# Optimization experiments

Hardware: AMD Instinct MI355X
Metric: run time of the kernel (lower is better)

Reference implementation:

```python
import jax, jax.numpy as jnp
import numpy as np

N = 100000
E = 1600000
D = 256

def setup_inputs() -> dict:
    key = jax.random.key(0)
    k1, k2, k3 = jax.random.split(key, 3)
    nodes = jax.random.normal(k1, (N, D), dtype=jnp.float32)
    edge_index = jax.random.randint(k2, (2, E), 0, N, dtype=jnp.int64)
    W = jax.random.normal(k3, (D, D), dtype=jnp.float32) * 0.05  # GCN lin weight [out,in]
    b = jnp.zeros((D,), dtype=jnp.float32)
    gamma = jnp.ones((D,), dtype=jnp.float32)
    beta = jnp.zeros((D,), dtype=jnp.float32)
    return {"nodes": nodes, "edge_index": edge_index, "W": W, "b": b,
            "gamma": gamma, "beta": beta}

def reference(nodes, edge_index, W, b, gamma, beta):
    n = nodes.shape[0]
    loop = jnp.arange(n, dtype=edge_index.dtype)
    src = jnp.concatenate([edge_index[0], loop])  # add self-loops (PyG default)
    dst = jnp.concatenate([edge_index[1], loop])
    # linear transform
    x = nodes @ W.T  # [N, D]
    # symmetric normalization: deg from target index, weight 1 per edge
    deg = jnp.zeros((n,), dtype=x.dtype).at[dst].add(1.0)
    dinv = jnp.where(deg > 0, jax.lax.rsqrt(deg), 0.0)
    norm = dinv[src] * dinv[dst]  # [E+N]
    msg = x[src] * norm[:, None]
    out = jax.ops.segment_sum(msg, dst, num_segments=n) + b  # [N, D]
    # LayerNorm over feature dim
    mu = jnp.mean(out, axis=-1, keepdims=True)
    var = jnp.mean(jnp.square(out - mu), axis=-1, keepdims=True)
    out = (out - mu) * jax.lax.rsqrt(var + 1e-5) * gamma + beta
    # ReLU; dropout is identity in eval mode
    return jax.nn.relu(out)
```

## Files before the change

### kernel.cpp

```cpp
#include <hip/hip_runtime.h>
#include <hip/hip_bf16.h>

#define NN 100000
#define EE 1600000
#define DD 256
#define CAP 64
#define NPART 391
#define ABLK 512
#define ACHUNK 3125

typedef __bf16 bf16x8 __attribute__((ext_vector_type(8)));
typedef float f32x4 __attribute__((ext_vector_type(4)));

__device__ __forceinline__ unsigned short f2bf(float f) {
    unsigned u = __builtin_bit_cast(unsigned, f);
    u += 0x7fffu + ((u >> 16) & 1u);
    return (unsigned short)(u >> 16);
}
__device__ __forceinline__ float bf2f(unsigned short h) {
    unsigned u = ((unsigned)h) << 16;
    return __builtin_bit_cast(float, u);
}

__global__ __launch_bounds__(256) void k_partA(const void* __restrict__ eptr,
        unsigned int* __restrict__ gseg2, int* __restrict__ cnts, int* __restrict__ pref) {
    __shared__ int lcnt[NPART];
    __shared__ int lcnt2[NPART];
    __shared__ int lpref[NPART];
    __shared__ int sA[512], sB[512];
    __shared__ int lflag;
    const int b = blockIdx.x, tid = threadIdx.x;
    if (tid == 0) lflag = 0;
    for (int i = tid; i < NPART; i += 256) { lcnt[i] = 0; lcnt2[i] = 0; }
    __syncthreads();
    if (tid < 64) {
        const unsigned long long w = ((const unsigned long long*)eptr)[tid];
        if (w > 0xFFFFFFFFULL) lflag = 1;
    }
    __syncthreads();
    const int is32 = lflag;
    const int e0 = b * ACHUNK;
    for (int e = e0 + tid; e < e0 + ACHUNK; e += 256) {
        const int d = is32 ? ((const int*)eptr)[EE + e]
                           : (int)((const long long*)eptr)[EE + e];
        atomicAdd(&lcnt[d >> 8], 1);
    }
    __syncthreads();
    sA[tid]       = (tid < NPART) ? lcnt[tid] : 0;
    sA[tid + 256] = (tid + 256 < NPART) ? lcnt[tid + 256] : 0;
    __syncthreads();
    int* s = sA; int* d2 = sB;
    for (int off = 1; off < 512; off <<= 1) {
        d2[tid]       = s[tid]       + (tid >= off ? s[tid - off] : 0);
        d2[tid + 256] = s[tid + 256] + (tid + 256 >= off ? s[tid + 256 - off] : 0);
        __syncthreads();
        int* t = s; s = d2; d2 = t;
    }
    for (int i = tid; i < NPART; i += 256) {
        lpref[i] = (i == 0) ? 0 : s[i - 1];
        cnts[(size_t)i * ABLK + b] = lcnt[i];
        pref[(size_t)i * ABLK + b] = (i == 0) ? 0 : s[i - 1];
    }
    __syncthreads();
    for (int e = e0 + tid; e < e0 + ACHUNK; e += 256) {
        int ss, dd;
        if (is32) { const int* p = (const int*)eptr; ss = p[e]; dd = p[EE + e]; }
        else { const long long* p = (const long long*)eptr; ss = (int)p[e]; dd = (int)p[EE + e]; }
        const int pp = dd >> 8;
        const int slot = atomicAdd(&lcnt2[pp], 1);
        gseg2[(size_t)b * ACHUNK + lpref[pp] + slot] = ((unsigned)ss << 8) | (unsigned)(dd & 255);
    }
}

__global__ __launch_bounds__(256) void k_partB(const unsigned int* __restrict__ gseg2,
        const int* __restrict__ cnts, const int* __restrict__ pref,
        int* __restrict__ bucket, int* __restrict__ cnt) {
    __shared__ int lc[256];
    __shared__ __align__(16) int lb[256 * CAP];
    const int p = blockIdx.x, tid = threadIdx.x;
    const int node0 = p * 256 + tid;
    lc[tid] = 1;
    lb[tid * CAP] = node0;
    __syncthreads();
    #pragma unroll
    for (int half = 0; half < 2; ++half) {
        const int bb = half * 256 + tid;
        const int c = cnts[(size_t)p * ABLK + bb];
        const unsigned int* seg = gseg2 + (size_t)bb * ACHUNK + pref[(size_t)p * ABLK + bb];
        for (int i = 0; i < c; ++i) {
            const unsigned int en = seg[i];
            const int d = en & 255;
            const int slot = atomicAdd(&lc[d], 1);
            if (slot < CAP) lb[d * CAP + slot] = (int)(en >> 8);
        }
    }
    __syncthreads();
    const size_t base = (size_t)p * 256 * CAP;
    #pragma unroll
    for (int it = 0; it < 16; ++it) {
        const int idx4 = it * 256 + tid;
        const int node = p * 256 + (idx4 >> 4);
        if (node < NN)
            *(uint4*)(bucket + base + (size_t)idx4 * 4) = *(const uint4*)&lb[idx4 * 4];
    }
    if (node0 < NN) cnt[node0] = lc[tid];
}

__global__ void k_detect(const unsigned long long* __restrict__ e64, int* __restrict__ flag) {
    if (threadIdx.x == 0 && blockIdx.x == 0) {
        int is32 = 0;
        for (int i = 0; i < 64; ++i)
            if (e64[i] > 0xFFFFFFFFULL) is32 = 1;
        *flag = is32;
    }
}
__global__ __launch_bounds__(256) void k_init(int* __restrict__ cnt, int* __restrict__ bucket) {
    int v = blockIdx.x * 256 + threadIdx.x;
    if (v < NN) { cnt[v] = 1; bucket[(size_t)v * CAP] = v; }
}
__global__ __launch_bounds__(256) void k_count_scatter(const void* __restrict__ eptr,
        const int* __restrict__ flag, int* __restrict__ cnt, int* __restrict__ bucket) {
    int e = blockIdx.x * 256 + threadIdx.x;
    if (e >= EE) return;
    int s, d;
    if (*flag) { const int* p = (const int*)eptr; s = p[e]; d = p[EE + e]; }
    else { const long long* p = (const long long*)eptr; s = (int)p[e]; d = (int)p[EE + e]; }
    int slot = atomicAdd(&cnt[d], 1);
    if (slot < CAP) bucket[(size_t)d * CAP + slot] = s;
}

__global__ __launch_bounds__(256) void k_wconv(const float* __restrict__ W,
        unsigned short* __restrict__ wf) {
    const int s = blockIdx.x * 256 + threadIdx.x;
    const int lane = s & 63;
    const int ks = (s >> 6) & 7;
    const int g  = (s >> 9) & 3;
    const int wv = s >> 11;
    const int feat = wv * 64 + g * 16 + (lane & 15);
    const int k0 = ks * 32 + (lane >> 4) * 8;
    const float* wp = W + (size_t)feat * 256 + k0;
    unsigned short o[8];
    #pragma unroll
    for (int j = 0; j < 8; ++j) o[j] = f2bf(wp[j]);
    uint4 pk;
    pk.x = o[0] | ((unsigned)o[1] << 16); pk.y = o[2] | ((unsigned)o[3] << 16);
    pk.z = o[4] | ((unsigned)o[5] << 16); pk.w = o[6] | ((unsigned)o[7] << 16);
    *(uint4*)(wf + (size_t)s * 8) = pk;
}

__global__ __launch_bounds__(256) void k_gemm(const float* __restrict__ nodes,
        const unsigned short* __restrict__ wf, const int* __restrict__ cnt,
        unsigned short* __restrict__ y) {
    __shared__ __align__(16) unsigned short xlds[64][264];
    const int tid = threadIdx.x, lane = tid & 63, wv = tid >> 6;
    const int q = lane >> 4, n0 = lane & 15;

    bf16x8 afrag[8][4];
    #pragma unroll
    for (int g = 0; g < 4; ++g)
        #pragma unroll
        for (int ks = 0; ks < 8; ++ks)
            afrag[ks][g] = *(const bf16x8*)(wf + ((((size_t)wv * 4 + g) * 8 + ks) * 64 + lane) * 8);

    const int row0 = blockIdx.x * 64;
    #pragma unroll
    for (int rr = 0; rr < 16; ++rr) {
        const int idx = rr * 256 + tid;
        const int r = idx >> 6, c4 = idx & 63;
        const int grow = min(row0 + r, NN - 1);
        const float4 v = *(const float4*)(nodes + (size_t)grow * 256 + c4 * 4);
        uint2 pk;
        pk.x = (unsigned)f2bf(v.x) | ((unsigned)f2bf(v.y) << 16);
        pk.y = (unsigned)f2bf(v.z) | ((unsigned)f2bf(v.w) << 16);
        *(uint2*)&xlds[r][c4 * 4] = pk;
    }
    __syncthreads();

    #pragma unroll
    for (int sub = 0; sub < 4; ++sub) {
        f32x4 acc[4] = {{0,0,0,0},{0,0,0,0},{0,0,0,0},{0,0,0,0}};
        #pragma unroll
        for (int ks = 0; ks < 8; ++ks) {
            const bf16x8 xf = *(const bf16x8*)&xlds[sub * 16 + n0][ks * 32 + q * 8];
            #pragma unroll
            for (int g = 0; g < 4; ++g)
                acc[g] = __builtin_amdgcn_mfma_f32_16x16x32_bf16(afrag[ks][g], xf, acc[g], 0, 0, 0);
        }
        const int node = row0 + sub * 16 + n0;
        if (node < NN) {
            const float dval = rsqrtf((float)cnt[node]);
            unsigned short* yp = y + (size_t)node * 256 + wv * 64 + q * 4;
            #pragma unroll
            for (int g = 0; g < 4; ++g) {
                uint2 pk;
                pk.x = (unsigned)f2bf(acc[g][0] * dval) | ((unsigned)f2bf(acc[g][1] * dval) << 16);
                pk.y = (unsigned)f2bf(acc[g][2] * dval) | ((unsigned)f2bf(acc[g][3] * dval) << 16);
                *(uint2*)(yp + g * 16) = pk;
            }
        }
    }
}

__global__ __launch_bounds__(256) void k_gather(const unsigned short* __restrict__ y,
        const int* __restrict__ cnt, const int* __restrict__ bucket,
        const float* __restrict__ bias, const float* __restrict__ gamma,
        const float* __restrict__ beta, float* __restrict__ out) {
    const int v = blockIdx.x * 4 + (threadIdx.x >> 6);
    const int lane = threadIdx.x & 63;
    const int h = lane >> 5, l = lane & 31;
    const int c = cnt[v];
    const int m = min(c, CAP);
    const int my = (lane < m) ? bucket[(size_t)v * CAP + lane] : 0;

    float acc[8] = {0, 0, 0, 0, 0, 0, 0, 0};
    #define ACCUM(P) do {                                                   \
        acc[0] += bf2f((unsigned short)((P).x & 0xffff));                   \
        acc[1] += bf2f((unsigned short)((P).x >> 16));                      \
        acc[2] += bf2f((unsigned short)((P).y & 0xffff));                   \
        acc[3] += bf2f((unsigned short)((P).y >> 16));                      \
        acc[4] += bf2f((unsigned short)((P).z & 0xffff));                   \
        acc[5] += bf2f((unsigned short)((P).z >> 16));                      \
        acc[6] += bf2f((unsigned short)((P).w & 0xffff));                   \
        acc[7] += bf2f((unsigned short)((P).w >> 16));                      \
    } while (0)

    int j = 0;
    for (; j + 8 <= m; j += 8) {
        const int s0 = __shfl(my, j + h);
        const int s1 = __shfl(my, j + 2 + h);
        const int s2 = __shfl(my, j + 4 + h);
        const int s3 = __shfl(my, j + 6 + h);
        const uint4 p0 = *((const uint4*)(y + (size_t)s0 * 256) + l);
        const uint4 p1 = *((const uint4*)(y + (size_t)s1 * 256) + l);
        const uint4 p2 = *((const uint4*)(y + (size_t)s2 * 256) + l);
        const uint4 p3 = *((const uint4*)(y + (size_t)s3 * 256) + l);
        ACCUM(p0); ACCUM(p1); ACCUM(p2); ACCUM(p3);
    }
    for (; j + 4 <= m; j += 4) {
        const int s0 = __shfl(my, j + h);
        const int s1 = __shfl(my, j + 2 + h);
        const uint4 p0 = *((const uint4*)(y + (size_t)s0 * 256) + l);
        const uint4 p1 = *((const uint4*)(y + (size_t)s1 * 256) + l);
        ACCUM(p0); ACCUM(p1);
    }
    for (; j + 2 <= m; j += 2) {
        const int s0 = __shfl(my, j + h);
        const uint4 p0 = *((const uint4*)(y + (size_t)s0 * 256) + l);
        ACCUM(p0);
    }
    if (j < m) {
        const int st = __shfl(my, j);
        if (h == 0) {
            const uint4 p0 = *((const uint4*)(y + (size_t)st * 256) + l);
            ACCUM(p0);
        }
    }
    #undef ACCUM

    #pragma unroll
    for (int i = 0; i < 8; ++i) acc[i] += __shfl_xor(acc[i], 32);

    const float dvv = rsqrtf((float)c);
    const float4 b0 = *(const float4*)(bias + l * 8);
    const float4 b1 = *(const float4*)(bias + l * 8 + 4);
    float u[8];
    u[0] = acc[0] * dvv + b0.x; u[1] = acc[1] * dvv + b0.y;
    u[2] = acc[2] * dvv + b0.z; u[3] = acc[3] * dvv + b0.w;
    u[4] = acc[4] * dvv + b1.x; u[5] = acc[5] * dvv + b1.y;
    u[6] = acc[6] * dvv + b1.z; u[7] = acc[7] * dvv + b1.w;

    float s1 = 0, s2 = 0;
    #pragma unroll
    for (int i = 0; i < 8; ++i) { s1 += u[i]; s2 += u[i] * u[i]; }
    #pragma unroll
    for (int o = 16; o > 0; o >>= 1) {
        s1 += __shfl_xor(s1, o);
        s2 += __shfl_xor(s2, o);
    }
    const float mean = s1 * (1.0f / 256.0f);
    const float var  = s2 * (1.0f / 256.0f) - mean * mean;
    const float rstd = rsqrtf(var + 1e-5f);

    const float4 g0 = *(const float4*)(gamma + l * 8);
    const float4 g1 = *(const float4*)(gamma + l * 8 + 4);
    const float4 e0 = *(const float4*)(beta + l * 8);
    const float4 e1 = *(const float4*)(beta + l * 8 + 4);
    float o8[8];
    o8[0] = fmaxf(0.0f, (u[0] - mean) * rstd * g0.x + e0.x);
    o8[1] = fmaxf(0.0f, (u[1] - mean) * rstd * g0.y + e0.y);
    o8[2] = fmaxf(0.0f, (u[2] - mean) * rstd * g0.z + e0.z);
    o8[3] = fmaxf(0.0f, (u[3] - mean) * rstd * g0.w + e0.w);
    o8[4] = fmaxf(0.0f, (u[4] - mean) * rstd * g1.x + e1.x);
    o8[5] = fmaxf(0.0f, (u[5] - mean) * rstd * g1.y + e1.y);
    o8[6] = fmaxf(0.0f, (u[6] - mean) * rstd * g1.z + e1.z);
    o8[7] = fmaxf(0.0f, (u[7] - mean) * rstd * g1.w + e1.w);
    float4 ov;
    if (h == 0) { ov.x = o8[0]; ov.y = o8[1]; ov.z = o8[2]; ov.w = o8[3]; }
    else        { ov.x = o8[4]; ov.y = o8[5]; ov.z = o8[6]; ov.w = o8[7]; }
    *(float4*)(out + (size_t)v * 256 + l * 8 + h * 4) = ov;
}

extern "C" void kernel_launch(void* const* d_in, const int* in_sizes, int n_in,
                              void* d_out, int out_size, void* d_ws, size_t ws_size,
                              hipStream_t stream) {
    const float* nodes = (const float*)d_in[0];
    const void*  edges = d_in[1];
    const float* W     = (const float*)d_in[2];
    const float* b     = (const float*)d_in[3];
    const float* gamma = (const float*)d_in[4];
    const float* beta  = (const float*)d_in[5];
    float* out = (float*)d_out;

    char* ws = (char*)d_ws;
    size_t off = 0;
    auto alloc = [&](size_t bytes) { size_t p = off; off = (off + bytes + 255) & ~(size_t)255; return p; };
    int*            cnt    = (int*)(ws + alloc((size_t)NN * 4));
    int*            flag   = (int*)(ws + alloc(256));
    int*            bucket = (int*)(ws + alloc((size_t)NN * CAP * 4));
    unsigned short* y      = (unsigned short*)(ws + alloc((size_t)NN * DD * 2));
    unsigned short* wf     = (unsigned short*)(ws + alloc((size_t)DD * DD * 2));
    int*            cnts   = (int*)(ws + alloc((size_t)NPART * ABLK * 4));
    int*            pref   = (int*)(ws + alloc((size_t)NPART * ABLK * 4));
    unsigned int*   gseg2  = (unsigned int*)(ws + alloc((size_t)EE * 4));
    const size_t full_need = off;
    (void)in_sizes; (void)n_in; (void)out_size;

    k_wconv<<<32, 256, 0, stream>>>(W, wf);
    if (ws_size >= full_need) {
        k_partA<<<ABLK, 256, 0, stream>>>(edges, gseg2, cnts, pref);
        k_partB<<<NPART, 256, 0, stream>>>(gseg2, cnts, pref, bucket, cnt);
    } else {
        k_detect<<<1, 64, 0, stream>>>((const unsigned long long*)edges, flag);
        k_init<<<(NN + 255) / 256, 256, 0, stream>>>(cnt, bucket);
        k_count_scatter<<<(EE + 255) / 256, 256, 0, stream>>>(edges, flag, cnt, bucket);
    }
    k_gemm<<<(NN + 63) / 64, 256, 0, stream>>>(nodes, wf, cnt, y);
    k_gather<<<NN / 4, 256, 0, stream>>>(y, cnt, bucket, b, gamma, beta, out);
}
```

Baseline: 374.5 us.

## Replace two-pass edge partition with global counting sort by destination partition

Splits the edge bucketing into histogram, column scan, partition prefix scan, sorted scatter, and per-partition bucket fill. Each partition's edges now sit contiguously, so bucket blocks read them with all threads striding coalesced. Before, each thread walked its own small per-chunk segment serially. Adds three kernel launches and a serial column scan of 512 steps per partition, and re-reads the edge list in the sort pass. Block indices are also remapped to chunks so that concurrently running blocks cover different parts of the edge array.

```diff
diff --git a/kernel.cpp b/kernel.cpp
--- a/kernel.cpp
+++ b/kernel.cpp
@@ -21,17 +21,15 @@
     unsigned u = ((unsigned)h) << 16;
     return __builtin_bit_cast(float, u);
 }
-
-__global__ __launch_bounds__(256) void k_partA(const void* __restrict__ eptr,
-        unsigned int* __restrict__ gseg2, int* __restrict__ cnts, int* __restrict__ pref) {
+__device__ __forceinline__ int chunk_of_block(int g) { return (g & 7) * 64 + (g >> 3); }
+
+__global__ __launch_bounds__(256) void k_hist(const void* __restrict__ eptr,
+        int* __restrict__ cnts ) {
     __shared__ int lcnt[NPART];
-    __shared__ int lcnt2[NPART];
-    __shared__ int lpref[NPART];
-    __shared__ int sA[512], sB[512];
     __shared__ int lflag;
-    const int b = blockIdx.x, tid = threadIdx.x;
+    const int b = chunk_of_block(blockIdx.x), tid = threadIdx.x;
     if (tid == 0) lflag = 0;
-    for (int i = tid; i < NPART; i += 256) { lcnt[i] = 0; lcnt2[i] = 0; }
+    for (int i = tid; i < NPART; i += 256) lcnt[i] = 0;
     __syncthreads();
     if (tid < 64) {
         const unsigned long long w = ((const unsigned long long*)eptr)[tid];
@@ -46,35 +44,68 @@
         atomicAdd(&lcnt[d >> 8], 1);
     }
     __syncthreads();
-    sA[tid]       = (tid < NPART) ? lcnt[tid] : 0;
-    sA[tid + 256] = (tid + 256 < NPART) ? lcnt[tid + 256] : 0;
-    __syncthreads();
-    int* s = sA; int* d2 = sB;
+    for (int i = tid; i < NPART; i += 256) cnts[(size_t)b * NPART + i] = lcnt[i];
+}
+
+__global__ __launch_bounds__(256) void k_colscan(const int* __restrict__ cnts,
+        int* __restrict__ gbase , int* __restrict__ T) {
+    const int p = blockIdx.x * 256 + threadIdx.x;
+    if (p >= NPART) return;
+    int run = 0;
+    #pragma unroll 8
+    for (int b = 0; b < ABLK; ++b) {
+        const int v = cnts[(size_t)b * NPART + p];
+        gbase[(size_t)b * NPART + p] = run;
+        run += v;
+    }
+    T[p] = run;
+}
+
+__global__ __launch_bounds__(512) void k_pscan(const int* __restrict__ T, int* __restrict__ P) {
+    __shared__ int sA[512], sB[512];
+    const int tid = threadIdx.x;
+    sA[tid] = (tid < NPART) ? T[tid] : 0;
+    __syncthreads();
+    int* s = sA; int* d = sB;
     for (int off = 1; off < 512; off <<= 1) {
-        d2[tid]       = s[tid]       + (tid >= off ? s[tid - off] : 0);
-        d2[tid + 256] = s[tid + 256] + (tid + 256 >= off ? s[tid + 256 - off] : 0);
+        d[tid] = s[tid] + (tid >= off ? s[tid - off] : 0);
         __syncthreads();
-        int* t = s; s = d2; d2 = t;
-    }
+        int* t = s; s = d; d = t;
+    }
+    if (tid <= NPART) P[tid] = (tid == 0) ? 0 : s[tid - 1];
+}
+
+__global__ __launch_bounds__(256) void k_sortwrite(const void* __restrict__ eptr,
+        const int* __restrict__ gbase, const int* __restrict__ P,
+        unsigned int* __restrict__ sorted) {
+    __shared__ int lc[NPART], gb[NPART];
+    __shared__ int lflag;
+    const int b = chunk_of_block(blockIdx.x), tid = threadIdx.x;
+    if (tid == 0) lflag = 0;
     for (int i = tid; i < NPART; i += 256) {
-        lpref[i] = (i == 0) ? 0 : s[i - 1];
-        cnts[(size_t)i * ABLK + b] = lcnt[i];
-        pref[(size_t)i * ABLK + b] = (i == 0) ? 0 : s[i - 1];
-    }
-    __syncthreads();
+        lc[i] = 0;
+        gb[i] = gbase[(size_t)b * NPART + i] + P[i];
+    }
+    __syncthreads();
+    if (tid < 64) {
+        const unsigned long long w = ((const unsigned long long*)eptr)[tid];
+        if (w > 0xFFFFFFFFULL) lflag = 1;
+    }
+    __syncthreads();
+    const int is32 = lflag;
+    const int e0 = b * ACHUNK;
     for (int e = e0 + tid; e < e0 + ACHUNK; e += 256) {
         int ss, dd;
         if (is32) { const int* p = (const int*)eptr; ss = p[e]; dd = p[EE + e]; }
         else { const long long* p = (const long long*)eptr; ss = (int)p[e]; dd = (int)p[EE + e]; }
         const int pp = dd >> 8;
-        const int slot = atomicAdd(&lcnt2[pp], 1);
-        gseg2[(size_t)b * ACHUNK + lpref[pp] + slot] = ((unsigned)ss << 8) | (unsigned)(dd & 255);
-    }
-}
-
-__global__ __launch_bounds__(256) void k_partB(const unsigned int* __restrict__ gseg2,
-        const int* __restrict__ cnts, const int* __restrict__ pref,
-        int* __restrict__ bucket, int* __restrict__ cnt) {
+        const int slot = atomicAdd(&lc[pp], 1);
+        sorted[gb[pp] + slot] = ((unsigned)ss << 8) | (unsigned)(dd & 255);
+    }
+}
+
+__global__ __launch_bounds__(256) void k_bucket(const unsigned int* __restrict__ sorted,
+        const int* __restrict__ P, int* __restrict__ bucket, int* __restrict__ cnt) {
     __shared__ int lc[256];
     __shared__ __align__(16) int lb[256 * CAP];
     const int p = blockIdx.x, tid = threadIdx.x;
@@ -82,17 +113,12 @@
     lc[tid] = 1;
     lb[tid * CAP] = node0;
     __syncthreads();
-    #pragma unroll
-    for (int half = 0; half < 2; ++half) {
-        const int bb = half * 256 + tid;
-        const int c = cnts[(size_t)p * ABLK + bb];
-        const unsigned int* seg = gseg2 + (size_t)bb * ACHUNK + pref[(size_t)p * ABLK + bb];
-        for (int i = 0; i < c; ++i) {
-            const unsigned int en = seg[i];
-            const int d = en & 255;
-            const int slot = atomicAdd(&lc[d], 1);
-            if (slot < CAP) lb[d * CAP + slot] = (int)(en >> 8);
-        }
+    const int start = P[p], end = P[p + 1];
+    for (int i = start + tid; i < end; i += 256) {
+        const unsigned int en = sorted[i];
+        const int d = en & 255;
+        const int slot = atomicAdd(&lc[d], 1);
+        if (slot < CAP) lb[d * CAP + slot] = (int)(en >> 8);
     }
     __syncthreads();
     const size_t base = (size_t)p * 256 * CAP;
@@ -319,16 +345,21 @@
     int*            bucket = (int*)(ws + alloc((size_t)NN * CAP * 4));
     unsigned short* y      = (unsigned short*)(ws + alloc((size_t)NN * DD * 2));
     unsigned short* wf     = (unsigned short*)(ws + alloc((size_t)DD * DD * 2));
-    int*            cnts   = (int*)(ws + alloc((size_t)NPART * ABLK * 4));
-    int*            pref   = (int*)(ws + alloc((size_t)NPART * ABLK * 4));
-    unsigned int*   gseg2  = (unsigned int*)(ws + alloc((size_t)EE * 4));
+    int*            cnts   = (int*)(ws + alloc((size_t)ABLK * NPART * 4));
+    int*            gbase  = (int*)(ws + alloc((size_t)ABLK * NPART * 4));
+    int*            T      = (int*)(ws + alloc(512 * 4));
+    int*            P      = (int*)(ws + alloc(512 * 4));
+    unsigned int*   sorted = (unsigned int*)(ws + alloc((size_t)EE * 4));
     const size_t full_need = off;
     (void)in_sizes; (void)n_in; (void)out_size;
 
     k_wconv<<<32, 256, 0, stream>>>(W, wf);
     if (ws_size >= full_need) {
-        k_partA<<<ABLK, 256, 0, stream>>>(edges, gseg2, cnts, pref);
-        k_partB<<<NPART, 256, 0, stream>>>(gseg2, cnts, pref, bucket, cnt);
+        k_hist<<<ABLK, 256, 0, stream>>>(edges, cnts);
+        k_colscan<<<2, 256, 0, stream>>>(cnts, gbase, T);
+        k_pscan<<<1, 512, 0, stream>>>(T, P);
+        k_sortwrite<<<ABLK, 256, 0, stream>>>(edges, gbase, P, sorted);
+        k_bucket<<<NPART, 256, 0, stream>>>(sorted, P, bucket, cnt);
     } else {
         k_detect<<<1, 64, 0, stream>>>((const unsigned long long*)edges, flag);
         k_init<<<(NN + 255) / 256, 256, 0, stream>>>(cnt, bucket);
```

Result: slower. 393.0 us (+4.9%).
